# Optimization experiments

Measured on AMD Instinct MI355X. Metric: run time of the kernel, lower is better.

Reference implementation:

```python
import jax, jax.numpy as jnp
import numpy as np

N, D, H = 4096, 1024, 2048


def positional_encoding(d_model, n):
    even_i = jnp.arange(0, d_model, 2, dtype=jnp.float32)
    denom = jnp.power(jnp.float32(10000.0), even_i / d_model)
    pos = jnp.arange(n, dtype=jnp.float32)[:, None]            # (N,1)
    even_pe = jnp.sin(pos / denom)                             # (N,D/2)
    odd_pe = jnp.cos(pos / denom)                              # (N,D/2)
    # interleave sin/cos: stack on axis 2 then flatten -> (N, D)
    return jnp.stack([even_pe, odd_pe], axis=2).reshape(n, d_model)


def setup_inputs() -> dict:
    key = jax.random.key(0)
    ks = jax.random.split(key, 5)
    X = jax.random.normal(ks[0], (N, D), dtype=jnp.float32)
    mask = jnp.ones((N,), dtype=jnp.int32)  # unused by the module
    Wv = jax.random.normal(ks[1], (D, D), dtype=jnp.float32) * 0.02
    bv = jnp.zeros((D,), dtype=jnp.float32)
    W1 = jax.random.normal(ks[2], (2 * D, H), dtype=jnp.float32) * 0.02
    b1 = jnp.zeros((H,), dtype=jnp.float32)
    W2 = jax.random.normal(ks[3], (H, N), dtype=jnp.float32) * 0.02
    b2 = jnp.zeros((N,), dtype=jnp.float32)
    return {"X": X, "mask": mask, "Wv": Wv, "bv": bv,
            "W1": W1, "b1": b1, "W2": W2, "b2": b2}


def reference(X, mask, Wv, bv, W1, b1, W2, b2):
    n, d = X.shape
    V = X @ Wv + bv                                            # (N,D)
    PE = positional_encoding(d, n).astype(X.dtype)
    E = PE * X                                                 # (N,D)
    # leave-one-out mean: (global sum - row_i) / (N-1)  [replaces O(N^2) loop]
    loo = (jnp.sum(E, axis=0, keepdims=True) - E) / (n - 1)    # (N,D)
    feat = jnp.concatenate([X, loo], axis=1)                   # (N,2D)
    hidden = jax.nn.relu(feat @ W1 + b1)                       # (N,H)
    att_scores = hidden @ W2 + b2                              # (N,N)
    att_weights = jax.nn.softmax(att_scores, axis=-1)          # (N,N)
    # dropout p=0 (inference) -> identity
    return att_weights @ V                                     # (N,D)
```

## Files before the change

### kernel.cpp

```cpp
#include <hip/hip_runtime.h>
#include <hip/hip_bf16.h>

#define TOK 4096
#define DIM 1024
#define HID 2048
#define LN10K 9.210340371976184f

typedef __bf16 bh;
typedef __bf16 v8bf __attribute__((ext_vector_type(8)));
typedef float v4f __attribute__((ext_vector_type(4)));

typedef const __attribute__((address_space(1))) void* gvp;
typedef __attribute__((address_space(3))) void* svp;

__device__ __forceinline__ void gl_lds16(const bh* g, bh* s) {
  __builtin_amdgcn_global_load_lds((gvp)g, (svp)s, 16, 0, 0);
}

__global__ __launch_bounds__(256) void prep_x_colsum(const float* __restrict__ X,
                                                     bh* __restrict__ featb,
                                                     float* __restrict__ S) {
  int cp = blockIdx.x * 256 + threadIdx.x;
  int c = cp * 2;
  int r0 = blockIdx.y * 16;
  float inv_denom = __expf(-(float)c * (LN10K / (float)DIM));
  float s0 = 0.f, s1 = 0.f;
#pragma unroll 4
  for (int r = r0; r < r0 + 16; ++r) {
    float2 x = *(const float2*)(X + (size_t)r * DIM + c);
    float sn, cs;
    __sincosf((float)r * inv_denom, &sn, &cs);
    s0 += sn * x.x;
    s1 += cs * x.y;
    bh pair[2] = {(bh)x.x, (bh)x.y};
    *(ushort2*)(featb + (size_t)r * (2 * DIM) + c) = *(ushort2*)pair;
  }
  atomicAdd(&S[c], s0);
  atomicAdd(&S[c + 1], s1);
}

__global__ __launch_bounds__(256) void prep_loo(const float* __restrict__ X,
                                                const float* __restrict__ S,
                                                bh* __restrict__ featb) {
  size_t e4 = ((size_t)blockIdx.x * 256 + threadIdx.x) * 4;
  int r = (int)(e4 >> 10);
  int c = (int)(e4 & 1023);
  float4 x = *(const float4*)(X + e4);
  float4 s = *(const float4*)(S + c);
  float id0 = __expf(-(float)c * (LN10K / (float)DIM));
  float id1 = __expf(-(float)(c + 2) * (LN10K / (float)DIM));
  float sn0, cs0, sn1, cs1;
  __sincosf((float)r * id0, &sn0, &cs0);
  __sincosf((float)r * id1, &sn1, &cs1);
  const float inv = 1.0f / (float)(TOK - 1);
  bh outv[4];
  outv[0] = (bh)((s.x - sn0 * x.x) * inv);
  outv[1] = (bh)((s.y - cs0 * x.y) * inv);
  outv[2] = (bh)((s.z - sn1 * x.z) * inv);
  outv[3] = (bh)((s.w - cs1 * x.w) * inv);
  *(ushort4*)(featb + (size_t)r * (2 * DIM) + DIM + c) = *(ushort4*)outv;
}

__global__ __launch_bounds__(256) void transpose_all(const float* __restrict__ Wv,
                                                     const float* __restrict__ W1,
                                                     const float* __restrict__ W2,
                                                     bh* __restrict__ WvT,
                                                     bh* __restrict__ W1T,
                                                     bh* __restrict__ W2T) {
  __shared__ float tile[32][33];
  int bid = blockIdx.x;
  const float* in; bh* out; int Ncol, R, bx, by;
  if (bid < 1024)      { in = Wv; out = WvT; Ncol = DIM; R = DIM;
                         bx = bid & 31; by = bid >> 5; }
  else if (bid < 5120) { int b = bid - 1024; in = W1; out = W1T; Ncol = HID; R = 2 * DIM;
                         bx = b & 63; by = b >> 6; }
  else                 { int b = bid - 5120; in = W2; out = W2T; Ncol = TOK; R = HID;
                         bx = b & 127; by = b >> 7; }
  int nb = bx * 32, rb = by * 32;
  int tx = threadIdx.x, ty = threadIdx.y;
#pragma unroll
  for (int j = 0; j < 32; j += 8)
    tile[ty + j][tx] = in[(size_t)(rb + ty + j) * Ncol + nb + tx];
  __syncthreads();
#pragma unroll
  for (int j = 0; j < 32; j += 8)
    out[(size_t)(nb + ty + j) * R + rb + tx] = (bh)tile[tx][ty + j];
}

template <int BN, bool RELU, bool TROUT, bool EXPS, typename OutT>
__global__ __launch_bounds__(256, 2) void gemm_bt(const bh* __restrict__ A,
                                                  const bh* __restrict__ BT,
                                                  const float* __restrict__ bias,
                                                  OutT* __restrict__ C,
                                                  float* __restrict__ rowsum,
                                                  int K, int lda, int ldbt, int ldc) {
  constexpr int NT = BN / 32;
  __shared__ bh As[128 * 64];
  __shared__ bh Bs[BN * 64];
  const int t = threadIdx.x;
  const int id = blockIdx.x;
  const int bm = (id & 31) * 128, bn = (id >> 5) * BN;

  const int srow = t >> 3;
  const int c8 = ((t & 7) ^ (srow & 7)) * 8;
  const bh* gA = A + (size_t)(bm + srow) * lda + c8;
  const bh* gB = BT + (size_t)(bn + srow) * ldbt + c8;
  bh* sA = As + t * 8;
  bh* sB = Bs + t * 8;

  const int lane = t & 63, w = t >> 6;
  const int wm = (w >> 1) * 64, wn = (w & 1) * (BN / 2);
  const int lc = lane & 15, q = lane >> 4;

  v4f acc[4][NT] = {};
  for (int k0 = 0; k0 < K; k0 += 64) {
#pragma unroll
    for (int j = 0; j < 4; ++j)
      gl_lds16(gA + k0 + j * 32 * lda, sA + j * 2048);
#pragma unroll
    for (int j = 0; j < BN / 32; ++j)
      gl_lds16(gB + k0 + j * 32 * ldbt, sB + j * 2048);
    __syncthreads();
#pragma unroll
    for (int h = 0; h < 2; ++h) {
      const int off = ((h * 4 + q) ^ (lc & 7)) * 8;
      v8bf af[4], bfr[NT];
#pragma unroll
      for (int mt = 0; mt < 4; ++mt)
        af[mt] = *(const v8bf*)(As + (wm + mt * 16 + lc) * 64 + off);
#pragma unroll
      for (int nt = 0; nt < NT; ++nt)
        bfr[nt] = *(const v8bf*)(Bs + (wn + nt * 16 + lc) * 64 + off);
#pragma unroll
      for (int mt = 0; mt < 4; ++mt)
#pragma unroll
        for (int nt = 0; nt < NT; ++nt)
          acc[mt][nt] = __builtin_amdgcn_mfma_f32_16x16x32_bf16(af[mt], bfr[nt], acc[mt][nt], 0, 0, 0);
    }
    __syncthreads();
  }

  const int r4 = q * 4;
  if (EXPS) {
    float bbv[NT];
#pragma unroll
    for (int nt = 0; nt < NT; ++nt)
      bbv[nt] = bias ? bias[bn + wn + nt * 16 + lc] : 0.0f;
#pragma unroll
    for (int mt = 0; mt < 4; ++mt) {
#pragma unroll
      for (int r = 0; r < 4; ++r) {
        int row = bm + wm + mt * 16 + r4 + r;
        float rs = 0.0f;
#pragma unroll
        for (int nt = 0; nt < NT; ++nt) {
          float val = __expf(acc[mt][nt][r] + bbv[nt]);
          rs += val;
          C[(size_t)row * ldc + bn + wn + nt * 16 + lc] = (OutT)val;
        }
        rs += __shfl_xor(rs, 1);
        rs += __shfl_xor(rs, 2);
        rs += __shfl_xor(rs, 4);
        rs += __shfl_xor(rs, 8);
        if (lc == 0) atomicAdd(rowsum + row, rs);
      }
    }
  } else if (TROUT) {
    bh* trs = As;
#pragma unroll
    for (int mt = 0; mt < 4; ++mt) {
#pragma unroll
      for (int nt = 0; nt < NT; ++nt) {
        int cl = wn + nt * 16 + lc;
        float bb = bias ? bias[bn + cl] : 0.0f;
#pragma unroll
        for (int r = 0; r < 4; ++r) {
          float val = acc[mt][nt][r] + bb;
          if (RELU) val = fmaxf(val, 0.0f);
          trs[cl * 128 + (wm + mt * 16 + r4 + r)] = (bh)val;
        }
      }
    }
    __syncthreads();
#pragma unroll
    for (int p = 0; p < 4; ++p) {
      int chunk = p * 256 + t;
      int vr = chunk >> 4, sc = chunk & 15;
      *(v8bf*)((bh*)C + (size_t)(bn + vr) * ldc + bm + sc * 8) =
          *(const v8bf*)(trs + vr * 128 + sc * 8);
    }
  } else {
#pragma unroll
    for (int mt = 0; mt < 4; ++mt) {
      int row0 = bm + wm + mt * 16 + r4;
#pragma unroll
      for (int nt = 0; nt < NT; ++nt) {
        int col = bn + wn + nt * 16 + lc;
        float bb = bias ? bias[col] : 0.0f;
#pragma unroll
        for (int r = 0; r < 4; ++r) {
          float val = acc[mt][nt][r] + bb;
          if (RELU) val = fmaxf(val, 0.0f);
          C[(size_t)(row0 + r) * ldc + col] = (OutT)val;
        }
      }
    }
  }
}

__global__ __launch_bounds__(256, 4) void gemm4_split(const bh* __restrict__ A,
                                                      const bh* __restrict__ BT,
                                                      float* __restrict__ C0,
                                                      float* __restrict__ C1) {
  __shared__ bh As[128 * 64];
  __shared__ bh Bs[128 * 64];
  const int t = threadIdx.x;
  const int id = blockIdx.x;
  const int bm = (id & 31) * 128, bn = (id >> 5) * 128;
  const int kbeg = blockIdx.y * (TOK / 2);

  const int sr = t >> 3;
  const int c8 = ((t & 7) ^ (sr & 7)) * 8;
  const bh* gA = A + (size_t)(bm + sr) * TOK + kbeg + c8;
  const bh* gB = BT + (size_t)(bn + sr) * TOK + kbeg + c8;
  bh* sA = As + t * 8;
  bh* sB = Bs + t * 8;

  const int lane = t & 63, w = t >> 6;
  const int wm = (w >> 1) * 64, wn = (w & 1) * 64;
  const int lc = lane & 15, q = lane >> 4;

  v4f acc[4][4] = {};
  for (int k0 = 0; k0 < TOK / 2; k0 += 64) {
#pragma unroll
    for (int j = 0; j < 4; ++j) {
      gl_lds16(gA + k0 + (size_t)(j * 32) * TOK, sA + j * 2048);
      gl_lds16(gB + k0 + (size_t)(j * 32) * TOK, sB + j * 2048);
    }
    __syncthreads();
#pragma unroll
    for (int h = 0; h < 2; ++h) {
      const int off = ((h * 4 + q) ^ (lc & 7)) * 8;
      v8bf af[4], bfr[4];
#pragma unroll
      for (int mt = 0; mt < 4; ++mt)
        af[mt] = *(const v8bf*)(As + (wm + mt * 16 + lc) * 64 + off);
#pragma unroll
      for (int nt = 0; nt < 4; ++nt)
        bfr[nt] = *(const v8bf*)(Bs + (wn + nt * 16 + lc) * 64 + off);
#pragma unroll
      for (int mt = 0; mt < 4; ++mt)
#pragma unroll
        for (int nt = 0; nt < 4; ++nt)
          acc[mt][nt] = __builtin_amdgcn_mfma_f32_16x16x32_bf16(af[mt], bfr[nt], acc[mt][nt], 0, 0, 0);
    }
    __syncthreads();
  }

  float* C = blockIdx.y ? C1 : C0;
  const int r4 = q * 4;
#pragma unroll
  for (int mt = 0; mt < 4; ++mt) {
    int row0 = bm + wm + mt * 16 + r4;
#pragma unroll
    for (int nt = 0; nt < 4; ++nt) {
      int col = bn + wn + nt * 16 + lc;
#pragma unroll
      for (int r = 0; r < 4; ++r)
        C[(size_t)(row0 + r) * DIM + col] = acc[mt][nt][r];
    }
  }
}

__global__ __launch_bounds__(256) void finalize(const float* __restrict__ p0,
                                                const float* __restrict__ p1,
                                                const float* __restrict__ rowsum,
                                                float* __restrict__ out) {
  size_t i = ((size_t)blockIdx.x * 256 + threadIdx.x) * 4;
  int row = (int)(i >> 10);
  float inv = 1.0f / rowsum[row];
  float4 a = *(const float4*)(p0 + i);
  float4 b = *(const float4*)(p1 + i);
  float4 o;
  o.x = (a.x + b.x) * inv; o.y = (a.y + b.y) * inv;
  o.z = (a.z + b.z) * inv; o.w = (a.w + b.w) * inv;
  *(float4*)(out + i) = o;
}

extern "C" void kernel_launch(void* const* d_in, const int* in_sizes, int n_in,
                              void* d_out, int out_size, void* d_ws, size_t ws_size,
                              hipStream_t stream) {
  (void)in_sizes; (void)n_in; (void)out_size; (void)ws_size;
  const float* X  = (const float*)d_in[0];
  const float* Wv = (const float*)d_in[2];
  const float* bv = (const float*)d_in[3];
  const float* W1 = (const float*)d_in[4];
  const float* b1 = (const float*)d_in[5];
  const float* W2 = (const float*)d_in[6];
  const float* b2 = (const float*)d_in[7];
  float* out = (float*)d_out;

  char* ws = (char*)d_ws;
  bh* featb = (bh*)(ws);
  bh* WvT   = (bh*)(ws + (16u << 20));
  bh* W1T   = (bh*)(ws + (18u << 20));
  bh* W2T   = (bh*)(ws + (26u << 20));
  bh* Vt    = (bh*)(ws + (42u << 20));
  bh* hid   = (bh*)(ws + (50u << 20));
  bh* scr   = (bh*)(ws + (66u << 20));
  float* S  = (float*)(ws + (98u << 20));
  float* rowsum = (float*)(ws + (98u << 20) + 4096);
  float* part0 = (float*)(ws);
  float* part1 = (float*)(ws + (26u << 20));

  hipError_t e = hipMemsetAsync(S, 0, 4096 + 4096 * sizeof(float), stream);
  (void)e;
  prep_x_colsum<<<dim3(DIM / 512, TOK / 16), 256, 0, stream>>>(X, featb, S);
  prep_loo<<<dim3((TOK * DIM) / 1024), 256, 0, stream>>>(X, S, featb);
  transpose_all<<<dim3(1024 + 4096 + 8192), dim3(32, 8), 0, stream>>>(
      Wv, W1, W2, WvT, W1T, W2T);

  gemm_bt<64, false, true, false, bh><<<dim3(32 * (DIM / 64)), 256, 0, stream>>>(
      featb, WvT, bv, Vt, nullptr, DIM, 2 * DIM, DIM, TOK);
  gemm_bt<128, true, false, false, bh><<<dim3(32 * (HID / 128)), 256, 0, stream>>>(
      featb, W1T, b1, hid, nullptr, 2 * DIM, 2 * DIM, 2 * DIM, HID);
  gemm_bt<128, false, false, true, bh><<<dim3(32 * (TOK / 128)), 256, 0, stream>>>(
      hid, W2T, b2, scr, rowsum, HID, HID, HID, TOK);
  gemm4_split<<<dim3(256, 2), 256, 0, stream>>>(scr, Vt, part0, part1);
  finalize<<<dim3((TOK * DIM) / 1024), 256, 0, stream>>>(part0, part1, rowsum, out);
}
```

Before: 312.1 us.

## Fuse final GEMM with softmax normalization and remap blocks across XCDs

Replaces the split-K final GEMM plus a separate finalize kernel with one kernel using 64x128 tiles over the full K, which applies the 1/rowsum normalization in the epilogue. This removes writing and rereading two fp32 partial buffers and one kernel launch. It also adds an XCD-aware block index remap to all GEMMs so neighbouring tiles land on the same XCD and share L2. In exchange, the smaller M tile lowers data reuse per block, and the kernel now relies on 512 blocks to fill the device instead of 512 split-K blocks.

```diff
diff --git a/kernel.cpp b/kernel.cpp
--- a/kernel.cpp
+++ b/kernel.cpp
@@ -15,6 +15,10 @@
 
 __device__ __forceinline__ void gl_lds16(const bh* g, bh* s) {
   __builtin_amdgcn_global_load_lds((gvp)g, (svp)s, 16, 0, 0);
+}
+
+__device__ __forceinline__ int xcd_remap(int id, int nwg) {
+  return (id & 7) * (nwg >> 3) + (id >> 3);
 }
 
 __global__ __launch_bounds__(256) void prep_x_colsum(const float* __restrict__ X,
@@ -98,7 +102,7 @@
   __shared__ bh As[128 * 64];
   __shared__ bh Bs[BN * 64];
   const int t = threadIdx.x;
-  const int id = blockIdx.x;
+  const int id = xcd_remap(blockIdx.x, gridDim.x);
   const int bm = (id & 31) * 128, bn = (id >> 5) * BN;
 
   const int srow = t >> 3;
@@ -208,48 +212,48 @@
   }
 }
 
-__global__ __launch_bounds__(256, 4) void gemm4_split(const bh* __restrict__ A,
+__global__ __launch_bounds__(256, 2) void gemm4_fused(const bh* __restrict__ A,
                                                       const bh* __restrict__ BT,
-                                                      float* __restrict__ C0,
-                                                      float* __restrict__ C1) {
-  __shared__ bh As[128 * 64];
+                                                      const float* __restrict__ rowsum,
+                                                      float* __restrict__ out) {
+  __shared__ bh As[64 * 64];
   __shared__ bh Bs[128 * 64];
   const int t = threadIdx.x;
-  const int id = blockIdx.x;
-  const int bm = (id & 31) * 128, bn = (id >> 5) * 128;
-  const int kbeg = blockIdx.y * (TOK / 2);
+  const int id = xcd_remap(blockIdx.x, gridDim.x);
+  const int bm = (id & 63) * 64, bn = (id >> 6) * 128;
 
   const int sr = t >> 3;
   const int c8 = ((t & 7) ^ (sr & 7)) * 8;
-  const bh* gA = A + (size_t)(bm + sr) * TOK + kbeg + c8;
-  const bh* gB = BT + (size_t)(bn + sr) * TOK + kbeg + c8;
+  const bh* gA = A + (size_t)(bm + sr) * TOK + c8;
+  const bh* gB = BT + (size_t)(bn + sr) * TOK + c8;
   bh* sA = As + t * 8;
   bh* sB = Bs + t * 8;
 
   const int lane = t & 63, w = t >> 6;
-  const int wm = (w >> 1) * 64, wn = (w & 1) * 64;
+  const int wm = (w >> 1) * 32, wn = (w & 1) * 64;
   const int lc = lane & 15, q = lane >> 4;
 
-  v4f acc[4][4] = {};
-  for (int k0 = 0; k0 < TOK / 2; k0 += 64) {
-#pragma unroll
-    for (int j = 0; j < 4; ++j) {
+  v4f acc[2][4] = {};
+  for (int k0 = 0; k0 < TOK; k0 += 64) {
+#pragma unroll
+    for (int j = 0; j < 2; ++j)
       gl_lds16(gA + k0 + (size_t)(j * 32) * TOK, sA + j * 2048);
+#pragma unroll
+    for (int j = 0; j < 4; ++j)
       gl_lds16(gB + k0 + (size_t)(j * 32) * TOK, sB + j * 2048);
-    }
     __syncthreads();
 #pragma unroll
     for (int h = 0; h < 2; ++h) {
       const int off = ((h * 4 + q) ^ (lc & 7)) * 8;
-      v8bf af[4], bfr[4];
-#pragma unroll
-      for (int mt = 0; mt < 4; ++mt)
+      v8bf af[2], bfr[4];
+#pragma unroll
+      for (int mt = 0; mt < 2; ++mt)
         af[mt] = *(const v8bf*)(As + (wm + mt * 16 + lc) * 64 + off);
 #pragma unroll
       for (int nt = 0; nt < 4; ++nt)
         bfr[nt] = *(const v8bf*)(Bs + (wn + nt * 16 + lc) * 64 + off);
 #pragma unroll
-      for (int mt = 0; mt < 4; ++mt)
+      for (int mt = 0; mt < 2; ++mt)
 #pragma unroll
         for (int nt = 0; nt < 4; ++nt)
           acc[mt][nt] = __builtin_amdgcn_mfma_f32_16x16x32_bf16(af[mt], bfr[nt], acc[mt][nt], 0, 0, 0);
@@ -257,34 +261,18 @@
     __syncthreads();
   }
 
-  float* C = blockIdx.y ? C1 : C0;
   const int r4 = q * 4;
 #pragma unroll
-  for (int mt = 0; mt < 4; ++mt) {
-    int row0 = bm + wm + mt * 16 + r4;
-#pragma unroll
-    for (int nt = 0; nt < 4; ++nt) {
-      int col = bn + wn + nt * 16 + lc;
-#pragma unroll
-      for (int r = 0; r < 4; ++r)
-        C[(size_t)(row0 + r) * DIM + col] = acc[mt][nt][r];
-    }
-  }
-}
-
-__global__ __launch_bounds__(256) void finalize(const float* __restrict__ p0,
-                                                const float* __restrict__ p1,
-                                                const float* __restrict__ rowsum,
-                                                float* __restrict__ out) {
-  size_t i = ((size_t)blockIdx.x * 256 + threadIdx.x) * 4;
-  int row = (int)(i >> 10);
-  float inv = 1.0f / rowsum[row];
-  float4 a = *(const float4*)(p0 + i);
-  float4 b = *(const float4*)(p1 + i);
-  float4 o;
-  o.x = (a.x + b.x) * inv; o.y = (a.y + b.y) * inv;
-  o.z = (a.z + b.z) * inv; o.w = (a.w + b.w) * inv;
-  *(float4*)(out + i) = o;
+  for (int mt = 0; mt < 2; ++mt) {
+#pragma unroll
+    for (int r = 0; r < 4; ++r) {
+      int row = bm + wm + mt * 16 + r4 + r;
+      float inv = 1.0f / rowsum[row];
+#pragma unroll
+      for (int nt = 0; nt < 4; ++nt)
+        out[(size_t)row * DIM + bn + wn + nt * 16 + lc] = acc[mt][nt][r] * inv;
+    }
+  }
 }
 
 extern "C" void kernel_launch(void* const* d_in, const int* in_sizes, int n_in,
@@ -310,8 +298,6 @@
   bh* scr   = (bh*)(ws + (66u << 20));
   float* S  = (float*)(ws + (98u << 20));
   float* rowsum = (float*)(ws + (98u << 20) + 4096);
-  float* part0 = (float*)(ws);
-  float* part1 = (float*)(ws + (26u << 20));
 
   hipError_t e = hipMemsetAsync(S, 0, 4096 + 4096 * sizeof(float), stream);
   (void)e;
@@ -326,6 +312,5 @@
       featb, W1T, b1, hid, nullptr, 2 * DIM, 2 * DIM, 2 * DIM, HID);
   gemm_bt<128, false, false, true, bh><<<dim3(32 * (TOK / 128)), 256, 0, stream>>>(
       hid, W2T, b2, scr, rowsum, HID, HID, HID, TOK);
-  gemm4_split<<<dim3(256, 2), 256, 0, stream>>>(scr, Vt, part0, part1);
-  finalize<<<dim3((TOK * DIM) / 1024), 256, 0, stream>>>(part0, part1, rowsum, out);
-}
+  gemm4_fused<<<dim3(512), 256, 0, stream>>>(scr, Vt, rowsum, out);
+}
```

Result: slower. 329.2 us (+5.5%).
